# Kernel tuning notes

Hardware: AMD Instinct MI355X
Metric: run time of the kernel (lower is better)

Reference implementation:

```python
import jax, jax.numpy as jnp
import numpy as np

D = 512; H = 8; DFF = 2048; S1 = 1024; S2 = 512; B = 8; EPS = 1e-5


def setup_inputs() -> dict:
    key = jax.random.key(0)
    ks = jax.random.split(key, 10)
    def w(k, shape):
        return jax.random.normal(k, shape, dtype=jnp.float32) * 0.02
    return {
        "rna_embed": jax.random.normal(ks[0], (S1, B, D), dtype=jnp.float32),
        "protein_embed": jax.random.normal(ks[1], (S2, B, D), dtype=jnp.float32),
        # self-attention params (torch MHA packed in_proj)
        "Wqkv_s": w(ks[2], (3 * D, D)), "bqkv_s": jnp.zeros((3 * D,), jnp.float32),
        "Wo_s": w(ks[3], (D, D)), "bo_s": jnp.zeros((D,), jnp.float32),
        # cross-attention params
        "Wqkv_c": w(ks[4], (3 * D, D)), "bqkv_c": jnp.zeros((3 * D,), jnp.float32),
        "Wo_c": w(ks[5], (D, D)), "bo_c": jnp.zeros((D,), jnp.float32),
        # FFN params
        "W1": w(ks[6], (DFF, D)), "b1": jnp.zeros((DFF,), jnp.float32),
        "W2": w(ks[7], (D, DFF)), "b2": jnp.zeros((D,), jnp.float32),
        # LayerNorm params: norm0_1, norm1_1, norm1_2, norm2
        "g0": jnp.ones((D,), jnp.float32), "be0": jnp.zeros((D,), jnp.float32),
        "g11": jnp.ones((D,), jnp.float32), "be11": jnp.zeros((D,), jnp.float32),
        "g12": jnp.ones((D,), jnp.float32), "be12": jnp.zeros((D,), jnp.float32),
        "g2": jnp.ones((D,), jnp.float32), "be2": jnp.zeros((D,), jnp.float32),
    }


def _layernorm(x, g, b):
    m = jnp.mean(x, axis=-1, keepdims=True)
    v = jnp.mean(jnp.square(x - m), axis=-1, keepdims=True)
    return (x - m) * jax.lax.rsqrt(v + EPS) * g + b


def _mha(xq, xkv, Wqkv, bqkv, Wo, bo):
    # xq: (Sq, B, D), xkv: (Sk, B, D)
    Wq, Wk, Wv = jnp.split(Wqkv, 3, axis=0)
    bq, bk, bv = jnp.split(bqkv, 3)
    hd = D // H
    scale = 1.0 / np.sqrt(hd).astype(np.float32)
    q = (xq @ Wq.T + bq).reshape(xq.shape[0], -1, H, hd)   # (Sq,B,H,hd)
    k = (xkv @ Wk.T + bk).reshape(xkv.shape[0], -1, H, hd)  # (Sk,B,H,hd)
    v = (xkv @ Wv.T + bv).reshape(xkv.shape[0], -1, H, hd)
    scores = jnp.einsum('qbhd,kbhd->bhqk', q, k) * scale    # (B,H,Sq,Sk)
    attn = jax.nn.softmax(scores, axis=-1)
    o = jnp.einsum('bhqk,kbhd->qbhd', attn, v).reshape(xq.shape[0], -1, D)
    return o @ Wo.T + bo


def reference(rna_embed, protein_embed, Wqkv_s, bqkv_s, Wo_s, bo_s,
              Wqkv_c, bqkv_c, Wo_c, bo_c, W1, b1, W2, b2,
              g0, be0, g11, be11, g12, be12, g2, be2):
    x1 = rna_embed
    # pre-norm self-attention
    h = _layernorm(x1, g0, be0)
    x1 = x1 + _mha(h, h, Wqkv_s, bqkv_s, Wo_s, bo_s)
    # pre-norm cross-attention (queries from x1, keys/values from protein)
    x1 = x1 + _mha(_layernorm(x1, g11, be11), _layernorm(protein_embed, g12, be12),
                   Wqkv_c, bqkv_c, Wo_c, bo_c)
    # pre-norm FFN
    h = _layernorm(x1, g2, be2)
    x1 = x1 + (jax.nn.relu(h @ W1.T + b1) @ W2.T + b2)
    return x1
```

## Files before the change

kernel.cpp:

```cpp
#include <hip/hip_runtime.h>

typedef unsigned short u16;
typedef unsigned int u32;
typedef u16 u16x8 __attribute__((ext_vector_type(8)));
typedef u16 u16x4 __attribute__((ext_vector_type(4)));
typedef short bfx8 __attribute__((ext_vector_type(8)));
typedef float f32x4 __attribute__((ext_vector_type(4)));

#define AS1 __attribute__((address_space(1)))
#define AS3 __attribute__((address_space(3)))

__device__ __forceinline__ u16 f2bf(float f) {
  union { float f; u32 u; } c; c.f = f;
  u32 u = c.u;
  u += 0x7fffu + ((u >> 16) & 1u);
  return (u16)(u >> 16);
}

__device__ __forceinline__ float bf2f(u16 b) {
  union { u32 u; float f; } c; c.u = ((u32)b) << 16;
  return c.f;
}

__device__ __forceinline__ u32 cvt_pk_bf16(float lo, float hi) {
  u32 r;
  asm("v_cvt_pk_bf16_f32 %0, %1, %2" : "=v"(r) : "v"(lo), "v"(hi));
  return r;
}

__device__ __forceinline__ float fexp2(float x) {
  float r;
  asm("v_exp_f32 %0, %1" : "=v"(r) : "v"(x));
  return r;
}

__device__ __forceinline__ void ln_core(float f[8], const float* __restrict__ g,
                                        const float* __restrict__ be,
                                        u16* __restrict__ out, int gw, int lane) {
  float s = 0.f, q = 0.f;
#pragma unroll
  for (int e = 0; e < 8; ++e) { s += f[e]; q += f[e] * f[e]; }
#pragma unroll
  for (int m = 1; m < 64; m <<= 1) { s += __shfl_xor(s, m); q += __shfl_xor(q, m); }
  float mean = s * (1.f / 512.f);
  float var = q * (1.f / 512.f) - mean * mean;
  float rs = rsqrtf(var + 1e-5f);
  const float4* g4 = (const float4*)g;
  const float4* b4 = (const float4*)be;
  float4 ga = g4[2 * lane], gb = g4[2 * lane + 1];
  float4 ba = b4[2 * lane], bb = b4[2 * lane + 1];
  float gv[8] = {ga.x, ga.y, ga.z, ga.w, gb.x, gb.y, gb.z, gb.w};
  float bv[8] = {ba.x, ba.y, ba.z, ba.w, bb.x, bb.y, bb.z, bb.w};
  u16x8 o;
#pragma unroll
  for (int e = 0; e < 8; ++e) o[e] = f2bf((f[e] - mean) * rs * gv[e] + bv[e]);
  ((u16x8*)(out + (size_t)gw * 512))[lane] = o;
}

__device__ __forceinline__ void ln_row_f32(const float* __restrict__ x, const float* __restrict__ g,
                                           const float* __restrict__ be, u16* __restrict__ out,
                                           int gw, int lane) {
  const float4* row = (const float4*)(x + (size_t)gw * 512);
  float4 a = row[2 * lane], b = row[2 * lane + 1];
  float f[8] = {a.x, a.y, a.z, a.w, b.x, b.y, b.z, b.w};
  ln_core(f, g, be, out, gw, lane);
}

__device__ __forceinline__ void ln_row_bf16(const u16* __restrict__ x, const float* __restrict__ g,
                                            const float* __restrict__ be, u16* __restrict__ out,
                                            int gw, int lane) {
  u16x8 v = ((const u16x8*)(x + (size_t)gw * 512))[lane];
  float f[8];
#pragma unroll
  for (int e = 0; e < 8; ++e) f[e] = bf2f(v[e]);
  ln_core(f, g, be, out, gw, lane);
}

__global__ __launch_bounds__(256) void cvtln_kernel(const float* __restrict__ a0, const float* __restrict__ a1,
                                                    const float* __restrict__ a2, const float* __restrict__ a3,
                                                    const float* __restrict__ a4, const float* __restrict__ a5,
                                                    u16* __restrict__ b0, u16* __restrict__ b1,
                                                    u16* __restrict__ b2, u16* __restrict__ b3,
                                                    u16* __restrict__ b4, u16* __restrict__ b5,
                                                    const float* __restrict__ x, const float* __restrict__ g,
                                                    const float* __restrict__ be, u16* __restrict__ lnout,
                                                    const float* __restrict__ xp, const float* __restrict__ gp,
                                                    const float* __restrict__ bep, u16* __restrict__ lnoutp) {
  if (blockIdx.x < 4096) {
    int i = blockIdx.x * 256 + threadIdx.x;
    const float* s; u16* d; int off;
    if      (i < 196608) { s = a0; d = b0; off = i; }
    else if (i < 262144) { s = a1; d = b1; off = i - 196608; }
    else if (i < 458752) { s = a2; d = b2; off = i - 262144; }
    else if (i < 524288) { s = a3; d = b3; off = i - 458752; }
    else if (i < 786432) { s = a4; d = b4; off = i - 524288; }
    else                 { s = a5; d = b5; off = i - 786432; }
    float4 v = ((const float4*)s)[off];
    u16x4 o;
    o[0] = f2bf(v.x); o[1] = f2bf(v.y); o[2] = f2bf(v.z); o[3] = f2bf(v.w);
    ((u16x4*)d)[off] = o;
  } else if (blockIdx.x < 6144) {
    int gw = ((blockIdx.x - 4096) * 256 + threadIdx.x) >> 6;
    ln_row_f32(x, g, be, lnout, gw, threadIdx.x & 63);
  } else {
    int gw = ((blockIdx.x - 6144) * 256 + threadIdx.x) >> 6;
    ln_row_f32(xp, gp, bep, lnoutp, gw, threadIdx.x & 63);
  }
}

__global__ __launch_bounds__(256) void lnb_kernel(const u16* __restrict__ x,
                                                  const float* __restrict__ g,
                                                  const float* __restrict__ be,
                                                  u16* __restrict__ out, int ntok) {
  int gw = (blockIdx.x * 256 + threadIdx.x) >> 6;
  if (gw >= ntok) return;
  ln_row_bf16(x, g, be, out, gw, threadIdx.x & 63);
}

__device__ __forceinline__ void vt_body(const u16* __restrict__ vB, u16* __restrict__ vt,
                                        int stride, int S, int xblk, int b, int h) {
  __shared__ u16 lt[64 * 68];
  const int t = threadIdx.x;
  const int sr = t >> 3, dc = (t & 7) * 8;
#pragma unroll
  for (int p = 0; p < 2; ++p) {
    int s = xblk * 64 + sr + p * 32;
    u16x8 v = *(const u16x8*)(vB + (size_t)(s * 8 + b) * stride + h * 64 + dc);
    u16x4 lo, hi;
    lo[0]=v[0]; lo[1]=v[1]; lo[2]=v[2]; lo[3]=v[3];
    hi[0]=v[4]; hi[1]=v[5]; hi[2]=v[6]; hi[3]=v[7];
    *(u16x4*)&lt[(sr + p * 32) * 68 + dc] = lo;
    *(u16x4*)&lt[(sr + p * 32) * 68 + dc + 4] = hi;
  }
  __syncthreads();
#pragma unroll
  for (int p = 0; p < 2; ++p) {
    int d = sr + p * 32;
    u16x8 o;
#pragma unroll
    for (int e = 0; e < 8; ++e) o[e] = lt[(dc + e) * 68 + d];
    *(u16x8*)(vt + ((size_t)(b * 8 + h) * 64 + d) * S + xblk * 64 + dc) = o;
  }
}

__global__ __launch_bounds__(256) void vt2_kernel(const u16* __restrict__ v0, u16* __restrict__ t0,
                                                  const u16* __restrict__ v1, u16* __restrict__ t1) {
  int id = blockIdx.x;
  if (id < 1024) {
    vt_body(v0, t0, 1536, 1024, id & 15, (id >> 4) & 7, id >> 7);
  } else {
    int l = id - 1024;
    vt_body(v1, t1, 1024, 512, l & 7, (l >> 3) & 7, l >> 6);
  }
}

template <int EPI, int BM, int BN, int WRg>
__device__ __forceinline__ void gemm8_body(const u16* __restrict__ A,
                                           const u16* __restrict__ Bw,
                                           const float* __restrict__ bias,
                                           const void* __restrict__ res,
                                           void* __restrict__ Cout,
                                           int M, int K, int bn, int bm,
                                           u16* __restrict__ lds) {
  constexpr int WCg = 8 / WRg;
  constexpr int RPW = BM / WRg;
  constexpr int IM = RPW / 16;
  constexpr int CPW = BN / WCg;
  constexpr int JN = CPW / 16;
  constexpr int LD = (BM + BN) / 64;
  u16* lA = lds;
  u16* lB = lds + 2 * BM * 64;
  const int tid = threadIdx.x;
  const int lane = tid & 63, w = tid >> 6;
  const int wr = w / WCg, wc = w % WCg;
  const int r15 = lane & 15, kg = lane >> 4;
  const int xr = (r15 & 7) << 4;

  f32x4 acc[IM][JN] = {};

  const int lrw = tid >> 3;
  const int lcl = ((tid & 7) * 8) ^ ((lrw & 7) * 8);
  const u16* gA = A + (size_t)(bn + lrw) * K + lcl;
  const u16* gB = Bw + (size_t)(bm + lrw) * K + lcl;
  const int ldsbase = (w * 8) * 64;

#define STAGE8(buf, t) do {                                                               \
    _Pragma("unroll")                                                                     \
    for (int i_ = 0; i_ < BM / 64; ++i_)                                                  \
      __builtin_amdgcn_global_load_lds((AS1 u32*)(gA + (size_t)(i_ * 64) * K + (t) * 64), \
                                       (AS3 u32*)&lA[(buf) * BM * 64 + i_ * 4096 + ldsbase], 16, 0, 0);\
    _Pragma("unroll")                                                                     \
    for (int i_ = 0; i_ < BN / 64; ++i_)                                                  \
      __builtin_amdgcn_global_load_lds((AS1 u32*)(gB + (size_t)(i_ * 64) * K + (t) * 64), \
                                       (AS3 u32*)&lB[(buf) * BN * 64 + i_ * 4096 + ldsbase], 16, 0, 0);\
  } while (0)

  const int nk = K >> 6;
  STAGE8(0, 0);
  for (int t = 0; t < nk; ++t) {
    const int cur = t & 1;
    if (t + 1 < nk) {
      STAGE8(cur ^ 1, t + 1);
      if constexpr (LD == 3)      asm volatile("s_waitcnt vmcnt(3)" ::: "memory");
      else if constexpr (LD == 4) asm volatile("s_waitcnt vmcnt(4)" ::: "memory");
      else                        asm volatile("s_waitcnt vmcnt(8)" ::: "memory");
    } else {
      asm volatile("s_waitcnt vmcnt(0)" ::: "memory");
    }
    __builtin_amdgcn_sched_barrier(0);
    __builtin_amdgcn_s_barrier();
    __builtin_amdgcn_sched_barrier(0);

    const char* Ac = (const char*)&lA[cur * BM * 64];
    const char* Bc = (const char*)&lB[cur * BN * 64];
    __builtin_amdgcn_s_setprio(1);
#pragma unroll
    for (int kk = 0; kk < 2; ++kk) {
      bfx8 a[IM], b[JN];
#pragma unroll
      for (int i = 0; i < IM; ++i)
        a[i] = *(const bfx8*)(Ac + (wr * RPW + i * 16 + r15) * 128 + ((kk * 64 + kg * 16) ^ xr));
#pragma unroll
      for (int j = 0; j < JN; ++j)
        b[j] = *(const bfx8*)(Bc + (wc * CPW + j * 16 + r15) * 128 + ((kk * 64 + kg * 16) ^ xr));
#pragma unroll
      for (int i = 0; i < IM; ++i)
#pragma unroll
        for (int j = 0; j < JN; ++j)
          acc[i][j] = __builtin_amdgcn_mfma_f32_16x16x32_bf16(a[i], b[j], acc[i][j], 0, 0, 0);
    }
    __builtin_amdgcn_s_setprio(0);
    __builtin_amdgcn_sched_barrier(0);
    __builtin_amdgcn_s_barrier();
  }
#undef STAGE8

#pragma unroll
  for (int i = 0; i < IM; ++i) {
#pragma unroll
    for (int j = 0; j < JN; ++j) {
      int col = bm + wc * CPW + j * 16 + r15;
      float bv = bias[col];
#pragma unroll
      for (int r = 0; r < 4; ++r) {
        int row = bn + wr * RPW + i * 16 + kg * 4 + r;
        size_t idx = (size_t)row * M + col;
        float v = acc[i][j][r] + bv;
        if (EPI == 1) v = fmaxf(v, 0.f);
        if (EPI == 3) {
          ((u16*)Cout)[idx] = f2bf(((const float*)res)[idx] + v);
        } else if (EPI == 4) {
          ((u16*)Cout)[idx] = f2bf(bf2f(((const u16*)res)[idx]) + v);
        } else if (EPI == 5) {
          ((float*)Cout)[idx] = bf2f(((const u16*)res)[idx]) + v;
        } else {
          ((u16*)Cout)[idx] = f2bf(v);
        }
      }
    }
  }
}

template <int EPI, int BM, int BN, int WRg, int MINW>
__global__ __launch_bounds__(512, MINW) void gemm8(const u16* __restrict__ A,
                                                   const u16* __restrict__ Bw,
                                                   const float* __restrict__ bias,
                                                   const void* __restrict__ res,
                                                   void* __restrict__ Cout,
                                                   int N, int M, int K) {
  __shared__ __align__(16) u16 lds[2 * (BM + BN) * 64];
  const int nwg = gridDim.x * gridDim.y;
  const int id = blockIdx.y * gridDim.x + blockIdx.x;
  const int swz = (id & 7) * (nwg >> 3) + (id >> 3);
  const int bn = (swz / gridDim.x) * BM;
  const int bm = (swz % gridDim.x) * BN;
  gemm8_body<EPI, BM, BN, WRg>(A, Bw, bias, res, Cout, M, K, bn, bm, lds);
}

__global__ __launch_bounds__(512, 4) void gemm_qkvkv(const u16* __restrict__ A0, const u16* __restrict__ W0,
                                                     const float* __restrict__ c0, u16* __restrict__ O0,
                                                     const u16* __restrict__ A1, const u16* __restrict__ W1,
                                                     const float* __restrict__ c1, u16* __restrict__ O1) {
  __shared__ __align__(16) u16 lds[2 * 256 * 64];
  const int id = blockIdx.x;
  if (id < 768) {
    const int swz = (id & 7) * 96 + (id >> 3);
    gemm8_body<0, 128, 128, 4>(A0, W0, c0, nullptr, O0, 1536, 512,
                               (swz / 12) * 128, (swz % 12) * 128, lds);
  } else {
    const int lid = id - 768;
    const int swz = (lid & 7) * 64 + (lid >> 3);
    gemm8_body<0, 64, 128, 2>(A1, W1, c1, nullptr, O1, 1024, 512,
                              (swz / 8) * 64, (swz % 8) * 128, lds);
  }
}

__global__ __launch_bounds__(512, 2) void attn_kernel(const u16* __restrict__ qB,
                                                      const u16* __restrict__ kB,
                                                      const u16* __restrict__ vtB,
                                                      u16* __restrict__ oB,
                                                      int qStride, int kvStride, int Sk) {
  __shared__ __align__(16) u16 lK[4][64 * 64];
  __shared__ __align__(16) u16 lVt[4][64 * 64];
  const int tid = threadIdx.x, lane = tid & 63, w = tid >> 6;
  const int sid = blockIdx.x;
  const int h = sid & 7, b = (sid >> 3) & 7, qt = sid >> 6;
  const int r15 = lane & 15, kg = lane >> 4;
  const int srow = lane >> 3;
  const int sxcol = ((lane & 7) * 8) ^ (srow * 8);

  const int q0 = qt * 256 + w * 32 + r15;
  const u16* qrow0 = qB + (size_t)(q0 * 8 + b) * qStride + h * 64;
  const u16* qrow1 = qB + (size_t)((q0 + 16) * 8 + b) * qStride + h * 64;
  bfx8 qf0a = *(const bfx8*)(qrow0 + kg * 8);
  bfx8 qf0b = *(const bfx8*)(qrow0 + 32 + kg * 8);
  bfx8 qf1a = *(const bfx8*)(qrow1 + kg * 8);
  bfx8 qf1b = *(const bfx8*)(qrow1 + 32 + kg * 8);

  const int rl = w * 8 + srow;
  const int krow = (rl & 32) | ((rl & 12) << 1) | ((rl & 16) >> 2) | (rl & 3);

  const u16* vbase = vtB + ((size_t)(b * 8 + h) * 64) * Sk;
  const u16* kp0 = kB + ((size_t)krow * 8 + b) * kvStride + h * 64 + sxcol;
  const size_t kAdv = (size_t)64 * 8 * kvStride;
  const u16* vp0 = vbase + (size_t)rl * Sk + sxcol;

#define STAGE(buf, tt) do {                                                           \
    __builtin_amdgcn_global_load_lds((AS1 u32*)(kp0 + (size_t)(tt) * kAdv),           \
                                     (AS3 u32*)&lK[buf][(w * 8) * 64], 16, 0, 0);     \
    __builtin_amdgcn_global_load_lds((AS1 u32*)(vp0 + (size_t)(tt) * 64),             \
                                     (AS3 u32*)&lVt[buf][(w * 8) * 64], 16, 0, 0);    \
  } while (0)

  const int nt = Sk / 64;
  const int np = nt >> 1;
  STAGE(0, 0); STAGE(1, 1);

  f32x4 oacc0[4] = {}, oacc1[4] = {};
  float mrow0 = -1e30f, mrow1 = -1e30f, lsum0 = 0.f, lsum1 = 0.f;
  const float C2 = 0.125f * 1.44269504088896340736f;
  const int xr = (r15 & 7) << 4;

  for (int i = 0; i < np; ++i) {
    __builtin_amdgcn_sched_barrier(0);
    __builtin_amdgcn_s_barrier();
    __builtin_amdgcn_sched_barrier(0);
    if (i + 1 < np) {
      const int sb = ((i + 1) & 1) * 2;
      STAGE(sb, 2 * (i + 1)); STAGE(sb + 1, 2 * (i + 1) + 1);
      asm volatile("s_waitcnt vmcnt(4)" ::: "memory");
    } else {
      asm volatile("s_waitcnt vmcnt(0)" ::: "memory");
    }
    __builtin_amdgcn_sched_barrier(0);

#pragma unroll
    for (int tb = 0; tb < 2; ++tb) {
      const int buf = (i & 1) * 2 + tb;
      const char* Kc = (const char*)lK[buf];
      const char* Vc = (const char*)lVt[buf];

      f32x4 s0[4] = {}, s1[4] = {};
      __builtin_amdgcn_s_setprio(1);
#pragma unroll
      for (int j = 0; j < 4; ++j) {
        const char* kp = Kc + (j * 16 + r15) * 128;
        bfx8 kf0 = *(const bfx8*)(kp + ((kg * 16) ^ xr));
        bfx8 kf1 = *(const bfx8*)(kp + ((64 + kg * 16) ^ xr));
        s0[j] = __builtin_amdgcn_mfma_f32_16x16x32_bf16(kf0, qf0a, s0[j], 0, 0, 0);
        s0[j] = __builtin_amdgcn_mfma_f32_16x16x32_bf16(kf1, qf0b, s0[j], 0, 0, 0);
        s1[j] = __builtin_amdgcn_mfma_f32_16x16x32_bf16(kf0, qf1a, s1[j], 0, 0, 0);
        s1[j] = __builtin_amdgcn_mfma_f32_16x16x32_bf16(kf1, qf1b, s1[j], 0, 0, 0);
      }
      __builtin_amdgcn_s_setprio(0);

      float lm0 = fmaxf(fmaxf(fmaxf(s0[0][0], s0[0][1]), fmaxf(s0[0][2], s0[0][3])),
                 fmaxf(fmaxf(fmaxf(s0[1][0], s0[1][1]), fmaxf(s0[1][2], s0[1][3])),
                 fmaxf(fmaxf(fmaxf(s0[2][0], s0[2][1]), fmaxf(s0[2][2], s0[2][3])),
                       fmaxf(fmaxf(s0[3][0], s0[3][1]), fmaxf(s0[3][2], s0[3][3])))));
      if (!__all(lm0 <= mrow0 + 16.0f)) {
        float m0 = fmaxf(lm0, __shfl_xor(lm0, 16));
        m0 = fmaxf(m0, __shfl_xor(m0, 32));
        float mn = fmaxf(mrow0, m0);
        float corr = fexp2((mrow0 - mn) * C2);
        mrow0 = mn;
        lsum0 *= corr;
#pragma unroll
        for (int jd = 0; jd < 4; ++jd)
#pragma unroll
          for (int r = 0; r < 4; ++r) oacc0[jd][r] *= corr;
      }
      float lm1 = fmaxf(fmaxf(fmaxf(s1[0][0], s1[0][1]), fmaxf(s1[0][2], s1[0][3])),
                 fmaxf(fmaxf(fmaxf(s1[1][0], s1[1][1]), fmaxf(s1[1][2], s1[1][3])),
                 fmaxf(fmaxf(fmaxf(s1[2][0], s1[2][1]), fmaxf(s1[2][2], s1[2][3])),
                       fmaxf(fmaxf(s1[3][0], s1[3][1]), fmaxf(s1[3][2], s1[3][3])))));
      if (!__all(lm1 <= mrow1 + 16.0f)) {
        float m1 = fmaxf(lm1, __shfl_xor(lm1, 16));
        m1 = fmaxf(m1, __shfl_xor(m1, 32));
        float mn = fmaxf(mrow1, m1);
        float corr = fexp2((mrow1 - mn) * C2);
        mrow1 = mn;
        lsum1 *= corr;
#pragma unroll
        for (int jd = 0; jd < 4; ++jd)
#pragma unroll
          for (int r = 0; r < 4; ++r) oacc1[jd][r] *= corr;
      }

      float bc0 = -mrow0 * C2, bc1 = -mrow1 * C2;
      float p0[4][4], p1[4][4];
      float ps0 = 0.f, ps1 = 0.f;
#pragma unroll
      for (int j = 0; j < 4; ++j)
#pragma unroll
        for (int r = 0; r < 4; ++r) {
          p0[j][r] = fexp2(fmaf(s0[j][r], C2, bc0));
          p1[j][r] = fexp2(fmaf(s1[j][r], C2, bc1));
          ps0 += p0[j][r]; ps1 += p1[j][r];
        }
      lsum0 += ps0; lsum1 += ps1;

      __builtin_amdgcn_s_setprio(1);
#pragma unroll
      for (int s2 = 0; s2 < 2; ++s2) {
        union { u32 u[4]; bfx8 v; } pt0, pt1;
        pt0.u[0] = cvt_pk_bf16(p0[2 * s2][0],     p0[2 * s2][1]);
        pt0.u[1] = cvt_pk_bf16(p0[2 * s2][2],     p0[2 * s2][3]);
        pt0.u[2] = cvt_pk_bf16(p0[2 * s2 + 1][0], p0[2 * s2 + 1][1]);
        pt0.u[3] = cvt_pk_bf16(p0[2 * s2 + 1][2], p0[2 * s2 + 1][3]);
        pt1.u[0] = cvt_pk_bf16(p1[2 * s2][0],     p1[2 * s2][1]);
        pt1.u[1] = cvt_pk_bf16(p1[2 * s2][2],     p1[2 * s2][3]);
        pt1.u[2] = cvt_pk_bf16(p1[2 * s2 + 1][0], p1[2 * s2 + 1][1]);
        pt1.u[3] = cvt_pk_bf16(p1[2 * s2 + 1][2], p1[2 * s2 + 1][3]);
#pragma unroll
        for (int jd = 0; jd < 4; ++jd) {
          const char* vp = Vc + (jd * 16 + r15) * 128;
          bfx8 vf = *(const bfx8*)(vp + ((s2 * 64 + kg * 16) ^ xr));
          oacc0[jd] = __builtin_amdgcn_mfma_f32_16x16x32_bf16(vf, pt0.v, oacc0[jd], 0, 0, 0);
          oacc1[jd] = __builtin_amdgcn_mfma_f32_16x16x32_bf16(vf, pt1.v, oacc1[jd], 0, 0, 0);
        }
      }
      __builtin_amdgcn_s_setprio(0);
    }
  }
#undef STAGE

  lsum0 += __shfl_xor(lsum0, 16);
  lsum0 += __shfl_xor(lsum0, 32);
  lsum1 += __shfl_xor(lsum1, 16);
  lsum1 += __shfl_xor(lsum1, 32);
  float inv0 = 1.f / lsum0, inv1 = 1.f / lsum1;
  u16* orow0 = oB + (size_t)(q0 * 8 + b) * 512 + h * 64;
  u16* orow1 = oB + (size_t)((q0 + 16) * 8 + b) * 512 + h * 64;
#pragma unroll
  for (int jd = 0; jd < 4; ++jd) {
    *(u32*)(orow0 + jd * 16 + kg * 4)     = cvt_pk_bf16(oacc0[jd][0] * inv0, oacc0[jd][1] * inv0);
    *(u32*)(orow0 + jd * 16 + kg * 4 + 2) = cvt_pk_bf16(oacc0[jd][2] * inv0, oacc0[jd][3] * inv0);
    *(u32*)(orow1 + jd * 16 + kg * 4)     = cvt_pk_bf16(oacc1[jd][0] * inv1, oacc1[jd][1] * inv1);
    *(u32*)(orow1 + jd * 16 + kg * 4 + 2) = cvt_pk_bf16(oacc1[jd][2] * inv1, oacc1[jd][3] * inv1);
  }
}

extern "C" void kernel_launch(void* const* d_in, const int* in_sizes, int n_in,
                              void* d_out, int out_size, void* d_ws, size_t ws_size,
                              hipStream_t stream) {
  const float* rna    = (const float*)d_in[0];
  const float* prot   = (const float*)d_in[1];
  const float* Wqkv_s = (const float*)d_in[2];
  const float* bqkv_s = (const float*)d_in[3];
  const float* Wo_s   = (const float*)d_in[4];
  const float* bo_s   = (const float*)d_in[5];
  const float* Wqkv_c = (const float*)d_in[6];
  const float* bqkv_c = (const float*)d_in[7];
  const float* Wo_c   = (const float*)d_in[8];
  const float* bo_c   = (const float*)d_in[9];
  const float* W1     = (const float*)d_in[10];
  const float* b1     = (const float*)d_in[11];
  const float* W2     = (const float*)d_in[12];
  const float* b2     = (const float*)d_in[13];
  const float* g0  = (const float*)d_in[14];
  const float* be0 = (const float*)d_in[15];
  const float* g11 = (const float*)d_in[16];
  const float* be11= (const float*)d_in[17];
  const float* g12 = (const float*)d_in[18];
  const float* be12= (const float*)d_in[19];
  const float* g2  = (const float*)d_in[20];
  const float* be2 = (const float*)d_in[21];
  float* out = (float*)d_out;

  u16* wbf      = (u16*)d_ws;
  u16* w_qkv_s  = wbf;
  u16* w_o_s    = wbf + 786432;
  u16* w_qkv_c  = wbf + 1048576;
  u16* w_o_c    = wbf + 1835008;
  u16* w_1      = wbf + 2097152;
  u16* w_2      = wbf + 3145728;
  u16* hbuf     = wbf + 4194304;
  u16* qkv      = hbuf + 4194304;
  u16* kvc      = qkv + 4194304;
  u16* attnO    = qkv + 12582912;
  u16* hp       = attnO + 4194304;
  u16* x1b      = hp + 2097152;
  u16* x1c      = x1b + 4194304;
  u16* ffnmid   = qkv;

  cvtln_kernel<<<7168, 256, 0, stream>>>(Wqkv_s, Wo_s, Wqkv_c, Wo_c, W1, W2,
                                         w_qkv_s, w_o_s, w_qkv_c, w_o_c, w_1, w_2,
                                         rna, g0, be0, hbuf, prot, g12, be12, hp);

  gemm_qkvkv<<<1280, 512, 0, stream>>>(hbuf, w_qkv_s, bqkv_s, qkv,
                                       hp, w_qkv_c + 512 * 512, bqkv_c + 512, kvc);

  vt2_kernel<<<1536, 256, 0, stream>>>(qkv + 1024, hbuf, kvc + 512, hp);

  attn_kernel<<<256, 512, 0, stream>>>(qkv, qkv + 512, hbuf, attnO, 1536, 1536, 1024);
  gemm8<3, 64, 128, 2, 6><<<dim3(4, 128), 512, 0, stream>>>(attnO, w_o_s, bo_s, rna, x1b, 8192, 512, 512);

  lnb_kernel<<<2048, 256, 0, stream>>>(x1b, g11, be11, hbuf, 8192);
  gemm8<0, 64, 128, 2, 6><<<dim3(4, 128), 512, 0, stream>>>(hbuf, w_qkv_c, bqkv_c, nullptr, qkv, 8192, 512, 512);
  attn_kernel<<<256, 512, 0, stream>>>(qkv, kvc, hp, attnO, 512, 1024, 512);
  gemm8<4, 64, 128, 2, 6><<<dim3(4, 128), 512, 0, stream>>>(attnO, w_o_c, bo_c, x1b, x1c, 8192, 512, 512);

  lnb_kernel<<<2048, 256, 0, stream>>>(x1c, g2, be2, hbuf, 8192);
  gemm8<1, 128, 128, 4, 4><<<dim3(16, 64), 512, 0, stream>>>(hbuf, w_1, b1, nullptr, ffnmid, 8192, 2048, 512);
  gemm8<5, 64, 128, 2, 6><<<dim3(4, 128), 512, 0, stream>>>(ffnmid, w_2, b2, x1c, out, 8192, 512, 2048);
}
```

Measured before the change: 174.0 us.

## Fuse post-residual LayerNorm into output-projection GEMMs via last-block atomic counters

```diff
diff --git a/kernel.cpp b/kernel.cpp
--- a/kernel.cpp
+++ b/kernel.cpp
@@ -63,16 +63,6 @@
   const float4* row = (const float4*)(x + (size_t)gw * 512);
   float4 a = row[2 * lane], b = row[2 * lane + 1];
   float f[8] = {a.x, a.y, a.z, a.w, b.x, b.y, b.z, b.w};
-  ln_core(f, g, be, out, gw, lane);
-}
-
-__device__ __forceinline__ void ln_row_bf16(const u16* __restrict__ x, const float* __restrict__ g,
-                                            const float* __restrict__ be, u16* __restrict__ out,
-                                            int gw, int lane) {
-  u16x8 v = ((const u16x8*)(x + (size_t)gw * 512))[lane];
-  float f[8];
-#pragma unroll
-  for (int e = 0; e < 8; ++e) f[e] = bf2f(v[e]);
   ln_core(f, g, be, out, gw, lane);
 }
 
@@ -108,15 +98,6 @@
   }
 }
 
-__global__ __launch_bounds__(256) void lnb_kernel(const u16* __restrict__ x,
-                                                  const float* __restrict__ g,
-                                                  const float* __restrict__ be,
-                                                  u16* __restrict__ out, int ntok) {
-  int gw = (blockIdx.x * 256 + threadIdx.x) >> 6;
-  if (gw >= ntok) return;
-  ln_row_bf16(x, g, be, out, gw, threadIdx.x & 63);
-}
-
 __device__ __forceinline__ void vt_body(const u16* __restrict__ vB, u16* __restrict__ vt,
                                         int stride, int S, int xblk, int b, int h) {
   __shared__ u16 lt[64 * 68];
@@ -161,7 +142,11 @@
                                            const void* __restrict__ res,
                                            void* __restrict__ Cout,
                                            int M, int K, int bn, int bm,
-                                           u16* __restrict__ lds) {
+                                           u16* __restrict__ lds,
+                                           const float* __restrict__ lng = nullptr,
+                                           const float* __restrict__ lnb = nullptr,
+                                           u16* __restrict__ lnout = nullptr,
+                                           u32* __restrict__ ctr = nullptr) {
   constexpr int WCg = 8 / WRg;
   constexpr int RPW = BM / WRg;
   constexpr int IM = RPW / 16;
@@ -247,9 +232,9 @@
         size_t idx = (size_t)row * M + col;
         float v = acc[i][j][r] + bv;
         if (EPI == 1) v = fmaxf(v, 0.f);
-        if (EPI == 3) {
+        if (EPI == 3 || EPI == 6) {
           ((u16*)Cout)[idx] = f2bf(((const float*)res)[idx] + v);
-        } else if (EPI == 4) {
+        } else if (EPI == 4 || EPI == 7) {
           ((u16*)Cout)[idx] = f2bf(bf2f(((const u16*)res)[idx]) + v);
         } else if (EPI == 5) {
           ((float*)Cout)[idx] = bf2f(((const u16*)res)[idx]) + v;
@@ -259,6 +244,51 @@
       }
     }
   }
+
+  if constexpr (EPI == 6 || EPI == 7) {
+    __shared__ u32 lastFlag;
+    __syncthreads();
+    if (tid == 0) {
+      __threadfence();
+      u32 old = atomicAdd(&ctr[bn >> 6], 1u);
+      lastFlag = ((old & 3u) == 3u) ? 1u : 0u;
+    }
+    __syncthreads();
+    if (lastFlag) {
+      __threadfence();
+      const int row = bn + (tid >> 3);
+      const int c0 = (tid & 7) * 64;
+      const u16* xr_ = (const u16*)Cout + (size_t)row * 512 + c0;
+      u16x8 xv[8];
+      float sum = 0.f, sq = 0.f;
+#pragma unroll
+      for (int c = 0; c < 8; ++c) {
+        xv[c] = *(const u16x8*)(xr_ + c * 8);
+#pragma unroll
+        for (int e = 0; e < 8; ++e) { float f = bf2f(xv[c][e]); sum += f; sq += f * f; }
+      }
+#pragma unroll
+      for (int m = 1; m < 8; m <<= 1) { sum += __shfl_xor(sum, m); sq += __shfl_xor(sq, m); }
+      float mean = sum * (1.f / 512.f);
+      float var = sq * (1.f / 512.f) - mean * mean;
+      float rs = rsqrtf(var + 1e-5f);
+      u16* orow = lnout + (size_t)row * 512 + c0;
+#pragma unroll
+      for (int c = 0; c < 8; ++c) {
+        float4 g0 = *(const float4*)(lng + c0 + c * 8);
+        float4 g1 = *(const float4*)(lng + c0 + c * 8 + 4);
+        float4 b0 = *(const float4*)(lnb + c0 + c * 8);
+        float4 b1 = *(const float4*)(lnb + c0 + c * 8 + 4);
+        float gv[8] = {g0.x, g0.y, g0.z, g0.w, g1.x, g1.y, g1.z, g1.w};
+        float bv[8] = {b0.x, b0.y, b0.z, b0.w, b1.x, b1.y, b1.z, b1.w};
+        u16x8 o;
+#pragma unroll
+        for (int e = 0; e < 8; ++e)
+          o[e] = f2bf((bf2f(xv[c][e]) - mean) * rs * gv[e] + bv[e]);
+        *(u16x8*)(orow + c * 8) = o;
+      }
+    }
+  }
 }
 
 template <int EPI, int BM, int BN, int WRg, int MINW>
@@ -267,14 +297,18 @@
                                                    const float* __restrict__ bias,
                                                    const void* __restrict__ res,
                                                    void* __restrict__ Cout,
-                                                   int N, int M, int K) {
+                                                   int N, int M, int K,
+                                                   const float* lng = nullptr,
+                                                   const float* lnb = nullptr,
+                                                   u16* lnout = nullptr,
+                                                   u32* ctr = nullptr) {
   __shared__ __align__(16) u16 lds[2 * (BM + BN) * 64];
   const int nwg = gridDim.x * gridDim.y;
   const int id = blockIdx.y * gridDim.x + blockIdx.x;
   const int swz = (id & 7) * (nwg >> 3) + (id >> 3);
   const int bn = (swz / gridDim.x) * BM;
   const int bm = (swz % gridDim.x) * BN;
-  gemm8_body<EPI, BM, BN, WRg>(A, Bw, bias, res, Cout, M, K, bn, bm, lds);
+  gemm8_body<EPI, BM, BN, WRg>(A, Bw, bias, res, Cout, M, K, bn, bm, lds, lng, lnb, lnout, ctr);
 }
 
 __global__ __launch_bounds__(512, 4) void gemm_qkvkv(const u16* __restrict__ A0, const u16* __restrict__ W0,
@@ -503,6 +537,8 @@
   u16* x1b      = hp + 2097152;
   u16* x1c      = x1b + 4194304;
   u16* ffnmid   = qkv;
+  u32* ctr0     = (u32*)(x1c + 4194304);
+  u32* ctr1     = ctr0 + 128;
 
   cvtln_kernel<<<7168, 256, 0, stream>>>(Wqkv_s, Wo_s, Wqkv_c, Wo_c, W1, W2,
                                          w_qkv_s, w_o_s, w_qkv_c, w_o_c, w_1, w_2,
@@ -514,14 +550,14 @@
   vt2_kernel<<<1536, 256, 0, stream>>>(qkv + 1024, hbuf, kvc + 512, hp);
 
   attn_kernel<<<256, 512, 0, stream>>>(qkv, qkv + 512, hbuf, attnO, 1536, 1536, 1024);
-  gemm8<3, 64, 128, 2, 6><<<dim3(4, 128), 512, 0, stream>>>(attnO, w_o_s, bo_s, rna, x1b, 8192, 512, 512);
-
-  lnb_kernel<<<2048, 256, 0, stream>>>(x1b, g11, be11, hbuf, 8192);
+  gemm8<6, 64, 128, 2, 6><<<dim3(4, 128), 512, 0, stream>>>(attnO, w_o_s, bo_s, rna, x1b,
+                                                            8192, 512, 512, g11, be11, hbuf, ctr0);
+
   gemm8<0, 64, 128, 2, 6><<<dim3(4, 128), 512, 0, stream>>>(hbuf, w_qkv_c, bqkv_c, nullptr, qkv, 8192, 512, 512);
   attn_kernel<<<256, 512, 0, stream>>>(qkv, kvc, hp, attnO, 512, 1024, 512);
-  gemm8<4, 64, 128, 2, 6><<<dim3(4, 128), 512, 0, stream>>>(attnO, w_o_c, bo_c, x1b, x1c, 8192, 512, 512);
-
-  lnb_kernel<<<2048, 256, 0, stream>>>(x1c, g2, be2, hbuf, 8192);
+  gemm8<7, 64, 128, 2, 6><<<dim3(4, 128), 512, 0, stream>>>(attnO, w_o_c, bo_c, x1b, x1c,
+                                                            8192, 512, 512, g2, be2, hbuf, ctr1);
+
   gemm8<1, 128, 128, 4, 4><<<dim3(16, 64), 512, 0, stream>>>(hbuf, w_1, b1, nullptr, ffnmid, 8192, 2048, 512);
   gemm8<5, 64, 128, 2, 6><<<dim3(4, 128), 512, 0, stream>>>(ffnmid, w_2, b2, x1c, out, 8192, 512, 2048);
 }
```

After: 281.1 us. 1.62x slower.
